# Performance work log

Hardware: AMD Instinct MI355X
Metric: run time of the kernel (lower is better)

The kernel has to match this reference:

```python
import jax, jax.numpy as jnp
import numpy as np

N, B, DIN = 128, 2, 128
D, DFF, NHEAD, NLAYERS = 256, 1024, 8, 2
BLOCK = 32
LENGTH = 160


def setup_inputs() -> dict:
    key = jax.random.key(0)
    ks = jax.random.split(key, 10)
    r = lambda k, sh: jax.random.normal(k, sh, jnp.float32) * 0.05
    return {
        "inputs": jax.random.normal(ks[0], (N, B, DIN), jnp.float32),
        "in_W1": r(ks[1], (DIN, DFF)), "in_b1": jnp.zeros((DFF,), jnp.float32),
        "in_W2": r(ks[2], (DFF, D)), "in_b2": jnp.zeros((D,), jnp.float32),
        "k_W1": r(ks[3], (DIN, DFF)), "k_b1": jnp.zeros((DFF,), jnp.float32),
        "k_W2": r(ks[4], (DFF, 2)), "k_b2": jnp.zeros((2,), jnp.float32),
        "Wqkv": r(ks[5], (NLAYERS, D, 3 * D)), "bqkv": jnp.zeros((NLAYERS, 3 * D), jnp.float32),
        "Wo": r(ks[6], (NLAYERS, D, D)), "bo": jnp.zeros((NLAYERS, D), jnp.float32),
        "ln1_g": jnp.ones((NLAYERS, D), jnp.float32), "ln1_b": jnp.zeros((NLAYERS, D), jnp.float32),
        "W1": r(ks[7], (NLAYERS, D, DFF)), "b1": jnp.zeros((NLAYERS, DFF), jnp.float32),
        "W2": r(ks[8], (NLAYERS, DFF, D)), "b2": jnp.zeros((NLAYERS, D), jnp.float32),
        "ln2_g": jnp.ones((NLAYERS, D), jnp.float32), "ln2_b": jnp.zeros((NLAYERS, D), jnp.float32),
        "length": LENGTH,
    }


def _ln(x, g, b):
    m = jnp.mean(x, axis=-1, keepdims=True)
    v = jnp.mean(jnp.square(x - m), axis=-1, keepdims=True)
    return (x - m) * jax.lax.rsqrt(v + 1e-5) * g + b


def _forward(inputs, in_W1, in_b1, in_W2, in_b2, k_W1, k_b1, k_W2, k_b2,
             Wqkv, bqkv, Wo, bo, ln1_g, ln1_b, W1, b1, W2, b2, ln2_g, ln2_b, length):
    n, b, din = inputs.shape
    d = in_W2.shape[1]
    H, dh = NHEAD, in_W2.shape[1] // NHEAD
    Wmax = 2 * BLOCK + 1
    L = length
    idx = jnp.arange(n)
    starts = jnp.maximum(0, idx - BLOCK)                 # [N]
    ends = jnp.minimum(L, idx + BLOCK + 1)               # [N]
    cols = starts[:, None] + jnp.arange(Wmax)[None, :]   # [N,Wmax] absolute column per window slot
    valid = cols < ends[:, None]                          # [N,Wmax] ragged-window mask

    # sinusoidal PE at absolute column positions (start_idx = max(0, i-block))
    pos = cols.astype(jnp.float32)
    div = jnp.exp(jnp.arange(0, din, 2, dtype=jnp.float32) * (-np.log(10000.0) / din))
    ang = pos[..., None] * div                            # [N,Wmax,din/2]
    pe = jnp.stack([jnp.sin(ang), jnp.cos(ang)], axis=-1).reshape(n, Wmax, din)

    # row token repeated across its window + PE, then input_ff
    x = inputs[:, None, :, :] + pe[:, :, None, :]         # [N,Wmax,B,din]
    h = jnp.maximum(x @ in_W1 + in_b1, 0.0) @ in_W2 + in_b2  # [N,Wmax,B,D]

    # TransformerEncoder (post-norm, relu, eval mode) over the window axis, padded slots masked as keys
    kmask = valid[:, None, None, None, :]                 # [N,1,1,1,Wmax]
    scale = 1.0 / np.sqrt(dh)
    for l in range(Wqkv.shape[0]):
        qkv = h @ Wqkv[l] + bqkv[l]
        q, k, v = [t.reshape(n, Wmax, b, H, dh) for t in jnp.split(qkv, 3, axis=-1)]
        s = jnp.einsum('nqbhe,nkbhe->nbhqk', q, k) * scale
        s = jnp.where(kmask, s, -jnp.inf)
        a = jax.nn.softmax(s, axis=-1)
        o = jnp.einsum('nbhqk,nkbhe->nqbhe', a, v).reshape(n, Wmax, b, d)
        h = _ln(h + o @ Wo[l] + bo[l], ln1_g[l], ln1_b[l])
        f = jnp.maximum(h @ W1[l] + b1[l], 0.0) @ W2[l] + b2[l]
        h = _ln(h + f, ln2_g[l], ln2_b[l])

    # hierarchy kernel scores (Gaussian band kernel with learned (mu, logsig) per row/batch)
    kp = jnp.maximum(inputs @ k_W1 + k_b1, 0.0) @ k_W2 + k_b2   # [N,B,2]
    hscale = L / n
    diff = cols.astype(jnp.float32) - idx[:, None].astype(jnp.float32) * hscale  # [N,Wmax]
    hier = -jnp.square(diff[:, :, None] - kp[:, None, :, 0]) * jnp.exp(kp[:, None, :, 1])  # [N,Wmax,B]

    # scatter banded values/scores into dense [N,L,...] then row-softmax and weighted combine
    n_idx = jnp.broadcast_to(idx[:, None], (n, Wmax))
    scat = jnp.where(valid, cols, L)                      # out-of-bounds -> dropped
    v_mat = jnp.zeros((n, L, b, d), jnp.float32).at[n_idx, scat].set(h, mode='drop')
    h_mat = jnp.full((n, L, b), -jnp.inf, jnp.float32).at[n_idx, scat].set(hier, mode='drop')
    w = jax.nn.softmax(h_mat, axis=0)[..., None]          # softmax over rows per column
    return jnp.sum(v_mat * w, axis=0)                     # [L,B,D]


def reference(inputs, in_W1, in_b1, in_W2, in_b2, k_W1, k_b1, k_W2, k_b2,
              Wqkv, bqkv, Wo, bo, ln1_g, ln1_b, W1, b1, W2, b2, ln2_g, ln2_b, length):
    return _forward(inputs, in_W1, in_b1, in_W2, in_b2, k_W1, k_b1, k_W2, k_b2,
                    Wqkv, bqkv, Wo, bo, ln1_g, ln1_b, W1, b1, W2, b2, ln2_g, ln2_b, length)
```

## Files before the change

### kernel.cpp

```cpp
#include <hip/hip_runtime.h>

constexpr int NN    = 128;
constexpr int BB    = 2;
constexpr int DIN   = 128;
constexpr int DD    = 256;
constexpr int DFF   = 1024;
constexpr int NH    = 8;
constexpr int DH    = 32;
constexpr int NL    = 2;
constexpr int BLK   = 32;
constexpr int WMAX  = 2 * BLK + 1;
constexpr int RROWS = NN * WMAX * BB;

typedef __attribute__((ext_vector_type(8))) short s16x8;
typedef __attribute__((ext_vector_type(4))) float f32x4;

__device__ __forceinline__ ushort f2bf(float f) {
  unsigned u = __float_as_uint(f);
  unsigned r = (u + 0x7fffu + ((u >> 16) & 1u)) >> 16;
  return (ushort)r;
}
__device__ __forceinline__ float bf2f(ushort h) {
  return __uint_as_float(((unsigned)h) << 16);
}

__device__ __forceinline__ void gld16(const void* g, void* l) {
  __builtin_amdgcn_global_load_lds(
      (const __attribute__((address_space(1))) void*)g,
      (__attribute__((address_space(3))) void*)l, 16, 0, 0);
}
__device__ __forceinline__ void vmdrain() {
  asm volatile("s_waitcnt vmcnt(0)" ::: "memory");
}

struct TD { const float* in; ushort* out; int K; int N; };
struct TPack { TD d[10]; };
constexpr int KP_BLOCKS   = NN * BB;
constexpr int WCONV_TILES = 1920;
constexpr int BX_BLOCKS   = RROWS * DIN / 256;

__global__ __launch_bounds__(256) void k_prep(
    TPack p, const float* __restrict__ inp, ushort* __restrict__ x,
    const float* __restrict__ kW1, const float* __restrict__ kb1,
    const float* __restrict__ kW2, const float* __restrict__ kb2,
    float* __restrict__ kp) {
  __shared__ float ls[32 * 33];
  int bid = blockIdx.x;
  int tid = threadIdx.x;
  if (bid < KP_BLOCKS) {
    int row = bid;
    float* xs = ls;
    float* red = ls + 256;
    if (tid < DIN) xs[tid] = inp[row * DIN + tid];
    __syncthreads();
    int j0 = tid * 4;
    float4 acc = *(const float4*)(kb1 + j0);
#pragma unroll 8
    for (int k = 0; k < DIN; ++k) {
      float xv = xs[k];
      float4 wv = *(const float4*)(kW1 + (size_t)k * DFF + j0);
      acc.x += xv * wv.x; acc.y += xv * wv.y;
      acc.z += xv * wv.z; acc.w += xv * wv.w;
    }
    acc.x = fmaxf(acc.x, 0.f); acc.y = fmaxf(acc.y, 0.f);
    acc.z = fmaxf(acc.z, 0.f); acc.w = fmaxf(acc.w, 0.f);
    float4 w2a = *(const float4*)(kW2 + 2 * j0);
    float4 w2b = *(const float4*)(kW2 + 2 * j0 + 4);
    float a0 = acc.x * w2a.x + acc.y * w2a.z + acc.z * w2b.x + acc.w * w2b.z;
    float a1 = acc.x * w2a.y + acc.y * w2a.w + acc.z * w2b.y + acc.w * w2b.w;
#pragma unroll
    for (int m = 32; m > 0; m >>= 1) {
      a0 += __shfl_xor(a0, m, 64);
      a1 += __shfl_xor(a1, m, 64);
    }
    if ((tid & 63) == 0) { red[(tid >> 6) * 2] = a0; red[(tid >> 6) * 2 + 1] = a1; }
    __syncthreads();
    if (tid == 0) {
      kp[row * 2 + 0] = red[0] + red[2] + red[4] + red[6] + kb2[0];
      kp[row * 2 + 1] = red[1] + red[3] + red[5] + red[7] + kb2[1];
    }
  } else if (bid < KP_BLOCKS + WCONV_TILES) {
    const int cum[11] = {0, 128, 384, 576, 768, 832, 896, 1152, 1408, 1664, 1920};
    int tb = bid - KP_BLOCKS;
    int mi = 0;
#pragma unroll
    for (int i = 0; i < 10; ++i) if (tb >= cum[i + 1]) mi = i + 1;
    TD t = p.d[mi];
    int tile = tb - cum[mi];
    int ntk = t.K >> 5;
    int tn = tile / ntk, tk = tile - tn * ntk;
    int r = tid >> 5, c = tid & 31;
#pragma unroll
    for (int i = 0; i < 4; ++i) {
      int kk = r + 8 * i;
      ls[kk * 33 + c] = t.in[(size_t)(tk * 32 + kk) * t.N + tn * 32 + c];
    }
    __syncthreads();
#pragma unroll
    for (int i = 0; i < 4; ++i) {
      int rr = r + 8 * i;
      t.out[(size_t)(tn * 32 + rr) * t.K + tk * 32 + c] = f2bf(ls[c * 33 + rr]);
    }
  } else {
    int e = (bid - KP_BLOCKS - WCONV_TILES) * 256 + tid;
    int i = e & 127, r = e >> 7;
    int n = r / (WMAX * BB);
    int rem = r - n * (WMAX * BB);
    int w = rem >> 1, b = rem & 1;
    int st = n - BLK; if (st < 0) st = 0;
    float pos = (float)(st + w);
    float div = __expf(-0.0719557841f * (float)(i & 126));
    float ang = pos * div;
    float pe = (i & 1) ? __cosf(ang) : __sinf(ang);
    x[e] = f2bf(inp[(n * BB + b) * DIN + i] + pe);
  }
}

template<int BMT, int RELU, int FUSE_LN, int BK>
__global__ __launch_bounds__(512) void k_gemm8(
    const ushort* __restrict__ A, const ushort* __restrict__ Bt,
    const float* __restrict__ bias, const ushort* __restrict__ resid,
    const float* __restrict__ lng, const float* __restrict__ lnb,
    ushort* __restrict__ out, int N, int K) {
  constexpr int MF   = BMT / 32;
  constexpr int CPR  = BK / 8;
  constexpr int ROWB = BK * 2;
  __shared__ __align__(16) char As[BMT * ROWB];
  __shared__ __align__(16) char Bs[256 * ROWB];
  int tid = threadIdx.x;
  int m0 = blockIdx.x * BMT, n0 = blockIdx.y * 256;
  int lane = tid & 63, w = tid >> 6;
  int wr = w >> 2, wc = w & 3;
  int fr = lane & 15, g = lane >> 4;
  f32x4 acc[MF][4] = {};

  for (int kb = 0; kb < K; kb += BK) {
    for (int e = tid; e < BMT * CPR; e += 512) {
      int row = e / CPR, c = e % CPR;
      gld16(A + (size_t)(m0 + row) * K + kb + ((c ^ (row & 7)) * 8), As + e * 16);
    }
    for (int e = tid; e < 256 * CPR; e += 512) {
      int row = e / CPR, c = e % CPR;
      gld16(Bt + (size_t)(n0 + row) * K + kb + ((c ^ (row & 7)) * 8), Bs + e * 16);
    }
    vmdrain();
    __syncthreads();
#pragma unroll
    for (int ks = 0; ks < BK / 32; ++ks) {
      int kByte = ks * 64 + g * 16;
      s16x8 a[MF], b[4];
#pragma unroll
      for (int m = 0; m < MF; ++m) {
        int row = wr * (BMT / 2) + m * 16 + fr;
        a[m] = *(const s16x8*)(As + ((row * ROWB + kByte) ^ ((row & 7) << 4)));
      }
#pragma unroll
      for (int n = 0; n < 4; ++n) {
        int row = wc * 64 + n * 16 + fr;
        b[n] = *(const s16x8*)(Bs + ((row * ROWB + kByte) ^ ((row & 7) << 4)));
      }
#pragma unroll
      for (int m = 0; m < MF; ++m)
#pragma unroll
        for (int n = 0; n < 4; ++n)
          acc[m][n] = __builtin_amdgcn_mfma_f32_16x16x32_bf16(a[m], b[n], acc[m][n], 0, 0, 0);
    }
    __syncthreads();
  }

  if constexpr (!FUSE_LN) {
#pragma unroll
    for (int m = 0; m < MF; ++m) {
      int rowb = m0 + wr * (BMT / 2) + m * 16 + g * 4;
#pragma unroll
      for (int n = 0; n < 4; ++n) {
        int col = n0 + wc * 64 + n * 16 + fr;
        float bv = bias[col];
#pragma unroll
        for (int j = 0; j < 4; ++j) {
          float v = acc[m][n][j] + bv;
          if (RELU) v = fmaxf(v, 0.f);
          out[(size_t)(rowb + j) * N + col] = f2bf(v);
        }
      }
    }
  } else {
    float* psum = (float*)As;
    float* psq  = (float*)(As + 4 * BMT * 4);
#pragma unroll
    for (int m = 0; m < MF; ++m) {
      int rowb = wr * (BMT / 2) + m * 16 + g * 4;
#pragma unroll
      for (int j = 0; j < 4; ++j) {
        float ps = 0.f, pq = 0.f;
#pragma unroll
        for (int n = 0; n < 4; ++n) {
          int col = wc * 64 + n * 16 + fr;
          float v = acc[m][n][j] + bias[col]
                  + bf2f(resid[(size_t)(m0 + rowb + j) * 256 + col]);
          acc[m][n][j] = v;
          ps += v; pq += v * v;
        }
#pragma unroll
        for (int d = 1; d < 16; d <<= 1) {
          ps += __shfl_xor(ps, d, 64);
          pq += __shfl_xor(pq, d, 64);
        }
        if (fr == 0) { psum[wc * BMT + rowb + j] = ps; psq[wc * BMT + rowb + j] = pq; }
      }
    }
    __syncthreads();
#pragma unroll
    for (int m = 0; m < MF; ++m) {
      int rowb = wr * (BMT / 2) + m * 16 + g * 4;
#pragma unroll
      for (int j = 0; j < 4; ++j) {
        int lr = rowb + j;
        float sm = psum[lr] + psum[BMT + lr] + psum[2 * BMT + lr] + psum[3 * BMT + lr];
        float sq = psq[lr] + psq[BMT + lr] + psq[2 * BMT + lr] + psq[3 * BMT + lr];
        float mean = sm * (1.f / 256.f);
        float var = sq * (1.f / 256.f) - mean * mean;
        float rs = rsqrtf(var + 1e-5f);
#pragma unroll
        for (int n = 0; n < 4; ++n) {
          int col = wc * 64 + n * 16 + fr;
          float v = (acc[m][n][j] - mean) * rs * lng[col] + lnb[col];
          out[(size_t)(m0 + lr) * 256 + col] = f2bf(v);
        }
      }
    }
  }
}

constexpr int QKS = 40;
constexpr int VTS = 104;
constexpr int PS  = 104;

__device__ __forceinline__ int vslot(int d, int r) {
  int rc = r >> 3;
  int sw = (rc < 8) ? (rc ^ (d >> 3)) : rc;
  return d * VTS + sw * 8 + (r & 7);
}

__global__ __launch_bounds__(320) void k_attn(
    const ushort* __restrict__ qkv, ushort* __restrict__ o,
    const int* __restrict__ lenp) {
  __shared__ __align__(16) ushort Ks[80 * QKS];
  __shared__ __align__(16) ushort Vt[32 * VTS];
  __shared__ __align__(16) ushort Pb[5 * 16 * PS];
  int L = lenp[0];
  int blk = blockIdx.x;
  int hh = blk & 7;
  int nb = blk >> 3;
  int b = nb & 1;
  int n = nb >> 1;
  int s0 = n - BLK; if (s0 < 0) s0 = 0;
  int e0 = n + BLK + 1; if (e0 > L) e0 = L;
  int vn = e0 - s0;
  int tid = threadIdx.x;

  for (int i = tid; i < 32 * VTS / 2; i += 320) ((uint*)Vt)[i] = 0;
  for (int i = tid; i < 15 * QKS / 2; i += 320)
    ((uint*)(Ks + 65 * QKS))[i] = 0;
  __syncthreads();
  for (int e = tid; e < 65 * 4; e += 320) {
    int r = e >> 2, c = e & 3;
    const ushort* base = qkv + ((size_t)(n * WMAX + r) * BB + b) * (3 * DD) + hh * DH;
    *(uint4*)(Ks + r * QKS + c * 8) = *(const uint4*)(base + DD + c * 8);
    uint4 vv = *(const uint4*)(base + 2 * DD + c * 8);
    const ushort* vp = (const ushort*)&vv;
#pragma unroll
    for (int u = 0; u < 8; ++u) Vt[vslot(c * 8 + u, r)] = vp[u];
  }

  int w = tid >> 6, lane = tid & 63;
  int fr = lane & 15, g = lane >> 4;
  int q0 = w * 16;
  ushort* Pw = Pb + w * 16 * PS;

  int qr_ld = q0 + fr; if (qr_ld > 64) qr_ld = 64;
  s16x8 aq = *(const s16x8*)(qkv + ((size_t)(n * WMAX + qr_ld) * BB + b) * (3 * DD)
                             + hh * DH + g * 8);
  __syncthreads();

  f32x4 sacc[5];
#pragma unroll
  for (int t = 0; t < 5; ++t) {
    s16x8 bk = *(const s16x8*)(Ks + (t * 16 + fr) * QKS + g * 8);
    f32x4 z = {0.f, 0.f, 0.f, 0.f};
    sacc[t] = __builtin_amdgcn_mfma_f32_16x16x32_bf16(aq, bk, z, 0, 0, 0);
  }
  const float scl = 0.17677669529663687f;
#pragma unroll
  for (int j = 0; j < 4; ++j) {
    float pv[5];
    float mx = -3e38f;
#pragma unroll
    for (int t = 0; t < 5; ++t) {
      bool ok = (t * 16 + fr) < vn;
      pv[t] = ok ? sacc[t][j] * scl : -3e38f;
      mx = fmaxf(mx, pv[t]);
    }
#pragma unroll
    for (int d = 1; d < 16; d <<= 1) mx = fmaxf(mx, __shfl_xor(mx, d, 64));
    float sum = 0.f;
#pragma unroll
    for (int t = 0; t < 5; ++t) {
      float e = ((t * 16 + fr) < vn) ? __expf(pv[t] - mx) : 0.f;
      pv[t] = e;
      sum += e;
    }
#pragma unroll
    for (int d = 1; d < 16; d <<= 1) sum += __shfl_xor(sum, d, 64);
    float inv = 1.f / sum;
#pragma unroll
    for (int t = 0; t < 5; ++t)
      Pw[(g * 4 + j) * PS + t * 16 + fr] = f2bf(pv[t] * inv);
  }
  {
    int zr = lane >> 2, zc = 80 + (lane & 3) * 4;
    *(uint2*)(Pw + zr * PS + zc) = make_uint2(0u, 0u);
  }
  __syncthreads();

  f32x4 oacc[2] = {};
#pragma unroll
  for (int k0 = 0; k0 < 3; ++k0) {
    s16x8 ap = *(const s16x8*)(Pw + fr * PS + k0 * 32 + g * 8);
#pragma unroll
    for (int nt = 0; nt < 2; ++nt) {
      s16x8 bv = *(const s16x8*)(Vt + vslot(nt * 16 + fr, k0 * 32 + g * 8));
      oacc[nt] = __builtin_amdgcn_mfma_f32_16x16x32_bf16(ap, bv, oacc[nt], 0, 0, 0);
    }
  }
#pragma unroll
  for (int nt = 0; nt < 2; ++nt) {
#pragma unroll
    for (int j = 0; j < 4; ++j) {
      int qr = q0 + g * 4 + j;
      if (qr < WMAX)
        o[((size_t)(n * WMAX + qr) * BB + b) * DD + hh * DH + nt * 16 + fr] =
            f2bf(oacc[nt][j]);
    }
  }
}

__global__ __launch_bounds__(256) void k_final(
    const ushort* __restrict__ h, const float* __restrict__ kp,
    float* __restrict__ out, const int* __restrict__ lenp) {
  int L = lenp[0];
  int t = blockIdx.x >> 1, b = blockIdx.x & 1;
  float hsc = (float)L / (float)NN;
  int nlo = t - BLK; if (nlo < 0) nlo = 0;
  int nhi = t + BLK; if (nhi > NN - 1) nhi = NN - 1;
  float mx = -3e38f;
  for (int n = nlo; n <= nhi; ++n) {
    float kp0 = kp[(n * BB + b) * 2 + 0];
    float kp1 = kp[(n * BB + b) * 2 + 1];
    float dif = (float)t - (float)n * hsc - kp0;
    float lg = -dif * dif * __expf(kp1);
    mx = fmaxf(mx, lg);
  }
  float sum = 0.f, acc = 0.f;
  int c = threadIdx.x;
  for (int n = nlo; n <= nhi; ++n) {
    float kp0 = kp[(n * BB + b) * 2 + 0];
    float kp1 = kp[(n * BB + b) * 2 + 1];
    float dif = (float)t - (float)n * hsc - kp0;
    float lg = -dif * dif * __expf(kp1);
    float p = __expf(lg - mx);
    sum += p;
    int st = n - BLK; if (st < 0) st = 0;
    int w = t - st;
    acc += p * bf2f(h[(size_t)((n * WMAX + w) * BB + b) * DD + c]);
  }
  out[(size_t)(t * BB + b) * DD + c] = acc / sum;
}

extern "C" void kernel_launch(void* const* d_in, const int* in_sizes, int n_in,
                              void* d_out, int out_size, void* d_ws, size_t ws_size,
                              hipStream_t stream) {
  const float* inputs = (const float*)d_in[0];
  const float* in_W1  = (const float*)d_in[1];
  const float* in_b1  = (const float*)d_in[2];
  const float* in_W2  = (const float*)d_in[3];
  const float* in_b2  = (const float*)d_in[4];
  const float* k_W1   = (const float*)d_in[5];
  const float* k_b1   = (const float*)d_in[6];
  const float* k_W2   = (const float*)d_in[7];
  const float* k_b2   = (const float*)d_in[8];
  const float* Wqkv   = (const float*)d_in[9];
  const float* bqkv   = (const float*)d_in[10];
  const float* Wo     = (const float*)d_in[11];
  const float* bo     = (const float*)d_in[12];
  const float* ln1_g  = (const float*)d_in[13];
  const float* ln1_b  = (const float*)d_in[14];
  const float* W1     = (const float*)d_in[15];
  const float* b1     = (const float*)d_in[16];
  const float* W2     = (const float*)d_in[17];
  const float* b2     = (const float*)d_in[18];
  const float* ln2_g  = (const float*)d_in[19];
  const float* ln2_b  = (const float*)d_in[20];
  const int*   lenp   = (const int*)d_in[21];
  float* out = (float*)d_out;
  (void)in_sizes; (void)n_in; (void)ws_size;

  ushort* wsu = (ushort*)d_ws;
  size_t off = 0;
  auto alloc = [&](size_t nelem) { ushort* p = wsu + off; off += (nelem + 7) & ~7ull; return p; };
  ushort* inW1t = alloc((size_t)DFF * DIN);
  ushort* inW2t = alloc((size_t)DD * DFF);
  ushort* Wqkvt = alloc((size_t)NL * 3 * DD * DD);
  ushort* Wot   = alloc((size_t)NL * DD * DD);
  ushort* W1t   = alloc((size_t)NL * DFF * DD);
  ushort* W2t   = alloc((size_t)NL * DD * DFF);
  ushort* x     = alloc((size_t)RROWS * DIN);
  ushort* tq    = alloc((size_t)RROWS * DFF);
  ushort* hb    = alloc((size_t)RROWS * DD);
  ushort* ob    = alloc((size_t)RROWS * DD);
  float*  kp    = (float*)(wsu + off);

  int L = out_size / (BB * DD);

  TPack tp;
  tp.d[0] = {in_W1, inW1t, DIN, DFF};
  tp.d[1] = {in_W2, inW2t, DFF, DD};
  tp.d[2] = {Wqkv,                        Wqkvt,                       DD, 3 * DD};
  tp.d[3] = {Wqkv + (size_t)DD * 3 * DD,  Wqkvt + (size_t)3 * DD * DD, DD, 3 * DD};
  tp.d[4] = {Wo,                    Wot,                   DD, DD};
  tp.d[5] = {Wo + (size_t)DD * DD,  Wot + (size_t)DD * DD, DD, DD};
  tp.d[6] = {W1,                      W1t,                    DD, DFF};
  tp.d[7] = {W1 + (size_t)DD * DFF,   W1t + (size_t)DFF * DD, DD, DFF};
  tp.d[8] = {W2,                      W2t,                    DFF, DD};
  tp.d[9] = {W2 + (size_t)DFF * DD,   W2t + (size_t)DD * DFF, DFF, DD};

  k_prep<<<KP_BLOCKS + WCONV_TILES + BX_BLOCKS, 256, 0, stream>>>(
      tp, inputs, x, k_W1, k_b1, k_W2, k_b2, kp);

  k_gemm8<128, 1, 0, 64><<<dim3(RROWS / 128, 4), 512, 0, stream>>>(
      x, inW1t, in_b1, nullptr, nullptr, nullptr, tq, DFF, DIN);
  k_gemm8<64, 0, 0, 128><<<dim3(RROWS / 64, 1), 512, 0, stream>>>(
      tq, inW2t, in_b2, nullptr, nullptr, nullptr, hb, DD, DFF);

  for (int l = 0; l < NL; ++l) {
    k_gemm8<128, 0, 0, 64><<<dim3(RROWS / 128, 3), 512, 0, stream>>>(
        hb, Wqkvt + (size_t)l * 3 * DD * DD, bqkv + (size_t)l * 3 * DD,
        nullptr, nullptr, nullptr, tq, 3 * DD, DD);
    k_attn<<<NN * BB * NH, 320, 0, stream>>>(tq, ob, lenp);
    k_gemm8<64, 0, 1, 128><<<dim3(RROWS / 64, 1), 512, 0, stream>>>(
        ob, Wot + (size_t)l * DD * DD, bo + (size_t)l * DD, hb,
        ln1_g + (size_t)l * DD, ln1_b + (size_t)l * DD, hb, DD, DD);
    k_gemm8<128, 1, 0, 64><<<dim3(RROWS / 128, 4), 512, 0, stream>>>(
        hb, W1t + (size_t)l * DFF * DD, b1 + (size_t)l * DFF,
        nullptr, nullptr, nullptr, tq, DFF, DD);
    k_gemm8<64, 0, 1, 128><<<dim3(RROWS / 64, 1), 512, 0, stream>>>(
        tq, W2t + (size_t)l * DD * DFF, b2 + (size_t)l * DD, hb,
        ln2_g + (size_t)l * DD, ln2_b + (size_t)l * DD, hb, DD, DFF);
  }
  k_final<<<L * BB, 256, 0, stream>>>(hb, kp, out, lenp);
}
```

Measured before the change: 262.8 us.

## Fuse positional-encoding input build into first input MLP GEMM

Removes the separate pass that wrote the bf16 PE-augmented input matrix x to global memory. A new GEMM kernel computes inputs+sinusoidal PE on the fly while staging A tiles into LDS, then runs MFMA with bias and ReLU. Attention block indexing is also reordered so the head index is the slow dimension. The cost is that PE transcendentals are recomputed once per N-tile (4x redundancy), and A loading is now synchronous compute instead of async global_load_lds.

After: 262.3 us (median of 2 runs). About the same (-0.2%).

```diff
diff --git a/kernel.cpp b/kernel.cpp
--- a/kernel.cpp
+++ b/kernel.cpp
@@ -37,10 +37,9 @@
 struct TPack { TD d[10]; };
 constexpr int KP_BLOCKS   = NN * BB;
 constexpr int WCONV_TILES = 1920;
-constexpr int BX_BLOCKS   = RROWS * DIN / 256;
 
 __global__ __launch_bounds__(256) void k_prep(
-    TPack p, const float* __restrict__ inp, ushort* __restrict__ x,
+    TPack p, const float* __restrict__ inp,
     const float* __restrict__ kW1, const float* __restrict__ kb1,
     const float* __restrict__ kW2, const float* __restrict__ kb2,
     float* __restrict__ kp) {
@@ -79,7 +78,7 @@
       kp[row * 2 + 0] = red[0] + red[2] + red[4] + red[6] + kb2[0];
       kp[row * 2 + 1] = red[1] + red[3] + red[5] + red[7] + kb2[1];
     }
-  } else if (bid < KP_BLOCKS + WCONV_TILES) {
+  } else {
     const int cum[11] = {0, 128, 384, 576, 768, 832, 896, 1152, 1408, 1664, 1920};
     int tb = bid - KP_BLOCKS;
     int mi = 0;
@@ -101,18 +100,81 @@
       int rr = r + 8 * i;
       t.out[(size_t)(tn * 32 + rr) * t.K + tk * 32 + c] = f2bf(ls[c * 33 + rr]);
     }
-  } else {
-    int e = (bid - KP_BLOCKS - WCONV_TILES) * 256 + tid;
-    int i = e & 127, r = e >> 7;
-    int n = r / (WMAX * BB);
-    int rem = r - n * (WMAX * BB);
-    int w = rem >> 1, b = rem & 1;
-    int st = n - BLK; if (st < 0) st = 0;
-    float pos = (float)(st + w);
-    float div = __expf(-0.0719557841f * (float)(i & 126));
-    float ang = pos * div;
-    float pe = (i & 1) ? __cosf(ang) : __sinf(ang);
-    x[e] = f2bf(inp[(n * BB + b) * DIN + i] + pe);
+  }
+}
+
+__global__ __launch_bounds__(512) void k_inmlp1(
+    const float* __restrict__ inp, const ushort* __restrict__ Bt,
+    const float* __restrict__ bias, ushort* __restrict__ out) {
+  __shared__ __align__(16) char As[128 * 128];
+  __shared__ __align__(16) char Bs[256 * 128];
+  int tid = threadIdx.x;
+  int m0 = blockIdx.x * 128, n0 = blockIdx.y * 256;
+  int lane = tid & 63, w = tid >> 6;
+  int wr = w >> 2, wc = w & 3;
+  int fr = lane & 15, g = lane >> 4;
+  f32x4 acc[4][4] = {};
+
+  for (int kb = 0; kb < DIN; kb += 64) {
+    for (int e = tid; e < 256 * 8; e += 512) {
+      int row = e >> 3, c = e & 7;
+      gld16(Bt + (size_t)(n0 + row) * DIN + kb + ((c ^ (row & 7)) * 8), Bs + e * 16);
+    }
+    for (int e = tid; e < 128 * 8; e += 512) {
+      int row = e >> 3, c = e & 7;
+      int r = m0 + row;
+      int n = r / (WMAX * BB);
+      int rem = r - n * (WMAX * BB);
+      int wn = rem >> 1, b = rem & 1;
+      int st = n - BLK; if (st < 0) st = 0;
+      float pos = (float)(st + wn);
+      const float* ip = inp + (n * BB + b) * DIN + kb + c * 8;
+      ushort vals[8];
+#pragma unroll
+      for (int u = 0; u < 8; ++u) {
+        int i = kb + c * 8 + u;
+        float div = __expf(-0.0719557841f * (float)(i & 126));
+        float ang = pos * div;
+        float pe = (i & 1) ? __cosf(ang) : __sinf(ang);
+        vals[u] = f2bf(ip[u] + pe);
+      }
+      *(uint4*)(As + ((row * 128 + c * 16) ^ ((row & 7) << 4))) = *(const uint4*)vals;
+    }
+    vmdrain();
+    __syncthreads();
+#pragma unroll
+    for (int ks = 0; ks < 2; ++ks) {
+      int kByte = ks * 64 + g * 16;
+      s16x8 a[4], b[4];
+#pragma unroll
+      for (int m = 0; m < 4; ++m) {
+        int row = wr * 64 + m * 16 + fr;
+        a[m] = *(const s16x8*)(As + ((row * 128 + kByte) ^ ((row & 7) << 4)));
+      }
+#pragma unroll
+      for (int n = 0; n < 4; ++n) {
+        int row = wc * 64 + n * 16 + fr;
+        b[n] = *(const s16x8*)(Bs + ((row * 128 + kByte) ^ ((row & 7) << 4)));
+      }
+#pragma unroll
+      for (int m = 0; m < 4; ++m)
+#pragma unroll
+        for (int n = 0; n < 4; ++n)
+          acc[m][n] = __builtin_amdgcn_mfma_f32_16x16x32_bf16(a[m], b[n], acc[m][n], 0, 0, 0);
+    }
+    __syncthreads();
+  }
+#pragma unroll
+  for (int m = 0; m < 4; ++m) {
+    int rowb = m0 + wr * 64 + m * 16 + g * 4;
+#pragma unroll
+    for (int n = 0; n < 4; ++n) {
+      int col = n0 + wc * 64 + n * 16 + fr;
+      float bv = bias[col];
+#pragma unroll
+      for (int j = 0; j < 4; ++j)
+        out[(size_t)(rowb + j) * DFF + col] = f2bf(fmaxf(acc[m][n][j] + bv, 0.f));
+    }
   }
 }
 
@@ -250,8 +312,8 @@
   __shared__ __align__(16) ushort Pb[5 * 16 * PS];
   int L = lenp[0];
   int blk = blockIdx.x;
-  int hh = blk & 7;
-  int nb = blk >> 3;
+  int hh = blk >> 8;
+  int nb = blk & 255;
   int b = nb & 1;
   int n = nb >> 1;
   int s0 = n - BLK; if (s0 < 0) s0 = 0;
@@ -414,7 +476,6 @@
   ushort* Wot   = alloc((size_t)NL * DD * DD);
   ushort* W1t   = alloc((size_t)NL * DFF * DD);
   ushort* W2t   = alloc((size_t)NL * DD * DFF);
-  ushort* x     = alloc((size_t)RROWS * DIN);
   ushort* tq    = alloc((size_t)RROWS * DFF);
   ushort* hb    = alloc((size_t)RROWS * DD);
   ushort* ob    = alloc((size_t)RROWS * DD);
@@ -434,11 +495,10 @@
   tp.d[8] = {W2,                      W2t,                    DFF, DD};
   tp.d[9] = {W2 + (size_t)DFF * DD,   W2t + (size_t)DD * DFF, DFF, DD};
 
-  k_prep<<<KP_BLOCKS + WCONV_TILES + BX_BLOCKS, 256, 0, stream>>>(
-      tp, inputs, x, k_W1, k_b1, k_W2, k_b2, kp);
-
-  k_gemm8<128, 1, 0, 64><<<dim3(RROWS / 128, 4), 512, 0, stream>>>(
-      x, inW1t, in_b1, nullptr, nullptr, nullptr, tq, DFF, DIN);
+  k_prep<<<KP_BLOCKS + WCONV_TILES, 256, 0, stream>>>(
+      tp, inputs, k_W1, k_b1, k_W2, k_b2, kp);
+
+  k_inmlp1<<<dim3(RROWS / 128, 4), 512, 0, stream>>>(inputs, inW1t, in_b1, tq);
   k_gemm8<64, 0, 0, 128><<<dim3(RROWS / 64, 1), 512, 0, stream>>>(
       tq, inW2t, in_b2, nullptr, nullptr, nullptr, hb, DD, DFF);
 
```
